# Performance work log

Measured on AMD Instinct MI355X. Metric: run time of the kernel, lower is better.

Reference implementation:

```python
import jax, jax.numpy as jnp
import numpy as np

NEG_INF = -9e15  # pygat masking constant
ALPHA = 0.2      # LeakyReLU slope


def _gat_head(h, adj_mask, W, a, concat):
    """One GraphAttentionLayer (pygat style).
    h: [b, N, Fin], adj_mask: [N, N] bool, W: [Fin, Fout], a: [2*Fout].
    """
    Fout = W.shape[1]
    Wh = jnp.einsum('bnf,fo->bno', h, W)              # [b, N, Fout]
    # e_ij = LeakyReLU(a_src . Wh_i + a_dst . Wh_j)
    e_src = Wh @ a[:Fout]                             # [b, N]
    e_dst = Wh @ a[Fout:]                             # [b, N]
    e = jax.nn.leaky_relu(e_src[:, :, None] + e_dst[:, None, :], ALPHA)  # [b, N, N]
    att = jax.nn.softmax(jnp.where(adj_mask, e, NEG_INF), axis=-1)
    out = jnp.einsum('bij,bjo->bio', att, Wh)         # [b, N, Fout]
    return jax.nn.elu(out) if concat else out


def setup_inputs() -> dict:
    key = jax.random.key(0)
    ks = jax.random.split(key, 8)
    b, N, F = 16384, 22, 192   # F = 3 * input_feature
    H = 192                    # 3 * hidden_feature (per head)
    x = jax.random.normal(ks[0], (b, N, F), dtype=jnp.float32)
    # symmetric binary adjacency with self loops (stand-in for skeleton graph A)
    u = jax.random.uniform(ks[1], (N, N))
    adj = ((u + u.T) < 0.8).astype(jnp.float32)
    adj = jnp.maximum(adj, jnp.eye(N, dtype=jnp.float32))
    s = 1.0 / np.sqrt(F)
    W1 = jax.random.normal(ks[2], (F, H), dtype=jnp.float32) * s
    a1 = jax.random.normal(ks[3], (2 * H,), dtype=jnp.float32) * s
    W2 = jax.random.normal(ks[4], (F, H), dtype=jnp.float32) * s
    a2 = jax.random.normal(ks[5], (2 * H,), dtype=jnp.float32) * s
    Wo = jax.random.normal(ks[6], (2 * H, F), dtype=jnp.float32) * (1.0 / np.sqrt(2 * H))
    ao = jax.random.normal(ks[7], (2 * F,), dtype=jnp.float32) * s
    return {"x": x, "adj": adj, "W1": W1, "a1": a1, "W2": W2, "a2": a2, "Wo": Wo, "ao": ao}


def reference(x, adj, W1, a1, W2, a2, Wo, ao):
    # ST_GCNA.forward: y = GAT(x_view, A) reshaped + residual x.
    # GAT (eval mode, dropout is identity): concat 2 heads, then elu(out_att).
    adj_mask = adj > 0
    h1 = _gat_head(x, adj_mask, W1, a1, concat=True)   # [b, N, H]
    h2 = _gat_head(x, adj_mask, W2, a2, concat=True)   # [b, N, H]
    hcat = jnp.concatenate([h1, h2], axis=-1)           # [b, N, 2H]
    y = jax.nn.elu(_gat_head(hcat, adj_mask, Wo, ao, concat=False))  # [b, N, F]
    return y + x
```

## Files before the change

kernel.cpp:

```cpp
#include <hip/hip_runtime.h>


typedef __attribute__((ext_vector_type(8))) short s16x8;
typedef __attribute__((ext_vector_type(4))) short s16x4;
typedef __attribute__((ext_vector_type(2))) int i32x2;
typedef __attribute__((ext_vector_type(4))) float f32x4;

constexpr int NN = 22;
constexpr int FF = 192;
constexpr int AS = 200;
constexpr int TS = 40;

__device__ __forceinline__ short f2bf(float f) {
  union { float f; unsigned u; } v; v.f = f;
  unsigned r = v.u + 0x7FFFu + ((v.u >> 16) & 1u);
  return (short)(r >> 16);
}

__device__ __forceinline__ int cvt_pk_bf16(float lo, float hi) {
  int r;
  asm("v_cvt_pk_bf16_f32 %0, %1, %2" : "=v"(r) : "v"(lo), "v"(hi));
  return r;
}

__device__ __forceinline__ float elu1(float v) {
  float e = __expf(v) - 1.0f;
  return v > 0.f ? v : e;
}

__global__ void prep_vec(const float* __restrict__ W1, const float* __restrict__ a1,
                         const float* __restrict__ W2, const float* __restrict__ a2,
                         const float* __restrict__ Wo, const float* __restrict__ ao,
                         float* __restrict__ vecs) {
  int t = blockIdx.x * 256 + threadIdx.x;
  if (t >= 1536) return;
  const float* W; const float* a; int k;
  if (t < 384)      { W = W1; k = t % 192;            a = a1 + (t / 192) * 192; }
  else if (t < 768) { int u = t - 384; W = W2; k = u % 192; a = a2 + (u / 192) * 192; }
  else              { int u = t - 768; W = Wo; k = u % 384; a = ao + (u / 384) * 192; }
  float s = 0.f;
  for (int o = 0; o < 192; ++o) s += W[k * 192 + o] * a[o];
  vecs[t] = s;
}

__global__ void prep_pack(const float* __restrict__ W1, const float* __restrict__ W2,
                          const float* __restrict__ Wo, const float* __restrict__ vecs,
                          short* __restrict__ dst) {
  int idx = blockIdx.x * 256 + threadIdx.x;
  const float* W; int off, ksteps, v0, v1;
  if (idx < 39936)      { W = W1; off = 0;     ksteps = 6;  v0 = 0;   v1 = 192;  }
  else if (idx < 79872) { W = W2; off = 39936; ksteps = 6;  v0 = 384; v1 = 576;  }
  else                  { W = Wo; off = 79872; ksteps = 12; v0 = 768; v1 = 1152; }
  int local = idx - off;
  int j = local & 7, l = (local >> 3) & 63, fi = local >> 9;
  int nt = fi / ksteps, ks = fi - nt * ksteps;
  int k = ks * 32 + ((l >> 4) << 3) + j;
  int nl = l & 15;
  float v;
  if (nt < 12) v = W[k * 192 + nt * 16 + nl];
  else         v = (nl == 0) ? vecs[v0 + k] : (nl == 1) ? vecs[v1 + k] : 0.f;
  dst[idx] = f2bf(v);
}

struct Accs { f32x4 a[2][3]; f32x4 e[2]; };

__device__ __forceinline__ void zacc(Accs& a) {
  #pragma unroll
  for (int m = 0; m < 2; ++m) {
    #pragma unroll
    for (int t = 0; t < 3; ++t) a.a[m][t] = (f32x4){0.f, 0.f, 0.f, 0.f};
    a.e[m] = (f32x4){0.f, 0.f, 0.f, 0.f};
  }
}

__device__ __attribute__((always_inline)) inline void gemm6(
    const short* A, const s16x8* __restrict__ B, int ksTot, int ksOff,
    Accs& ac, int m0, int kg, int wave, int lane) {
  for (int ks = 0; ks < 6; ++ks) {
    const short* ap = A + ks * 32 + kg * 8;
    s16x8 av0 = *(const s16x8*)(ap + m0 * AS);
    s16x8 av1 = *(const s16x8*)(ap + (m0 + 16) * AS);
    #pragma unroll
    for (int t = 0; t < 3; ++t) {
      s16x8 bv = B[((wave * 3 + t) * ksTot + ksOff + ks) * 64 + lane];
      ac.a[0][t] = __builtin_amdgcn_mfma_f32_16x16x32_bf16(av0, bv, ac.a[0][t], 0, 0, 0);
      ac.a[1][t] = __builtin_amdgcn_mfma_f32_16x16x32_bf16(av1, bv, ac.a[1][t], 0, 0, 0);
    }
    if (wave == 3) {
      s16x8 bv = B[(12 * ksTot + ksOff + ks) * 64 + lane];
      ac.e[0] = __builtin_amdgcn_mfma_f32_16x16x32_bf16(av0, bv, ac.e[0], 0, 0, 0);
      ac.e[1] = __builtin_amdgcn_mfma_f32_16x16x32_bf16(av1, bv, ac.e[1], 0, 0, 0);
    }
  }
}

__device__ __attribute__((always_inline)) inline void storeD(
    const Accs& ac, short* WhTp, float* esp, float* edp, int m0, int kg, int wave) {
  #pragma unroll
  for (int m = 0; m < 2; ++m)
    #pragma unroll
    for (int t = 0; t < 3; ++t) {
      int col = (wave * 3 + t) * 16 + m0;
      int row0 = m * 16 + kg * 4;
      i32x2 p = { cvt_pk_bf16(ac.a[m][t][0], ac.a[m][t][1]),
                  cvt_pk_bf16(ac.a[m][t][2], ac.a[m][t][3]) };
      *(i32x2*)&WhTp[col * TS + row0] = p;
    }
  if (wave == 3 && m0 < 2) {
    float* dst = m0 ? edp : esp;
    #pragma unroll
    for (int m = 0; m < 2; ++m) {
      int row0 = m * 16 + kg * 4;
      #pragma unroll
      for (int r = 0; r < 4; ++r)
        if (row0 + r < NN) dst[row0 + r] = ac.e[m][r];
    }
  }
}

__device__ __forceinline__ void softmax22(
    const float* es, const float* ed, const unsigned* adjm, short* attA, int tid) {
  int i = tid >> 3, jl = tid & 7;
  if (i >= NN) return;
  unsigned msk = adjm[i];
  float esi = es[i];
  float pv[3]; float mx = -3e38f;
  #pragma unroll
  for (int c = 0; c < 3; ++c) {
    int j = jl + 8 * c;
    int jc = j < NN ? j : 0;
    float e = esi + ed[jc];
    e = e > 0.f ? e : 0.2f * e;
    bool live = (j < NN) && ((msk >> j) & 1u);
    pv[c] = live ? e : -9e15f;
    mx = fmaxf(mx, pv[c]);
  }
  #pragma unroll
  for (int d = 1; d < 8; d <<= 1) mx = fmaxf(mx, __shfl_xor(mx, d, 8));
  float s = 0.f;
  #pragma unroll
  for (int c = 0; c < 3; ++c) { float q = __expf(pv[c] - mx); pv[c] = q; s += q; }
  #pragma unroll
  for (int d = 1; d < 8; d <<= 1) s += __shfl_xor(s, d, 8);
  float inv = 1.f / s;
  #pragma unroll
  for (int c = 0; c < 3; ++c) {
    int j = jl + 8 * c;
    if (j < 24) attA[i * TS + j] = (j < NN) ? f2bf(pv[c] * inv) : (short)0;
  }
  attA[i * TS + 24 + jl] = 0;
}

__device__ __attribute__((always_inline)) inline void pv22(
    const short* attAp, const short* WhTp, f32x4 pa[2][3], int m0, int kg, int wave) {
  s16x8 av0 = *(const s16x8*)(attAp + m0 * TS + kg * 8);
  s16x8 av1 = *(const s16x8*)(attAp + (m0 + 16) * TS + kg * 8);
  #pragma unroll
  for (int t = 0; t < 3; ++t) {
    int col = (wave * 3 + t) * 16 + m0;
    s16x8 bv = *(const s16x8*)(WhTp + col * TS + kg * 8);
    pa[0][t] = __builtin_amdgcn_mfma_f32_16x16x32_bf16(av0, bv, pa[0][t], 0, 0, 0);
    pa[1][t] = __builtin_amdgcn_mfma_f32_16x16x32_bf16(av1, bv, pa[1][t], 0, 0, 0);
  }
}

__global__ __launch_bounds__(256, 3) void gat_main(
    const float* __restrict__ x, const float* __restrict__ adj,
    const short* __restrict__ wsb, float* __restrict__ out) {
  __shared__ __align__(16) short As1[32 * AS];
  __shared__ __align__(16) short Ah [32 * AS];
  __shared__ __align__(16) short attA[32 * TS];
  __shared__ __align__(16) short WhT[FF * TS];
  __shared__ float es[NN], ed[NN];
  __shared__ unsigned adjm[NN];

  const int tid = threadIdx.x, lane = tid & 63, wave = tid >> 6;
  const int m0 = lane & 15, kg = (lane >> 4) & 3;
  const size_t b = blockIdx.x;
  const float* xb = x + b * (size_t)(NN * FF);

  for (int i4 = tid; i4 < 1056; i4 += 256) {
    int row = i4 / 48, c = (i4 - row * 48) * 4;
    float4 v = ((const float4*)xb)[i4];
    i32x2 p = { cvt_pk_bf16(v.x, v.y), cvt_pk_bf16(v.z, v.w) };
    *(i32x2*)&As1[row * AS + c] = p;
  }
  {
    int* z1 = (int*)(As1 + NN * AS);
    int* z2 = (int*)(Ah + NN * AS);
    for (int i = tid; i < 1000; i += 256) { z1[i] = 0; z2[i] = 0; }
  }
  if (tid < NN) {
    unsigned m = 0;
    for (int j = 0; j < NN; ++j) m |= (adj[tid * NN + j] > 0.f ? 1u : 0u) << j;
    adjm[tid] = m;
  }
  __syncthreads();

  const s16x8* BW  = (const s16x8*)wsb;
  const s16x8* BWo = (const s16x8*)wsb + 9984;

  Accs aco; zacc(aco);

  for (int h = 0; h < 2; ++h) {
    Accs ach; zacc(ach);
    gemm6(As1, BW + h * 4992, 6, 0, ach, m0, kg, wave, lane);
    storeD(ach, WhT, es, ed, m0, kg, wave);
    __syncthreads();

    softmax22(es, ed, adjm, attA, tid);
    __syncthreads();

    f32x4 pa[2][3];
    #pragma unroll
    for (int m = 0; m < 2; ++m)
      #pragma unroll
      for (int t = 0; t < 3; ++t) pa[m][t] = (f32x4){0.f, 0.f, 0.f, 0.f};
    pv22(attA, WhT, pa, m0, kg, wave);
    #pragma unroll
    for (int m = 0; m < 2; ++m)
      #pragma unroll
      for (int t = 0; t < 3; ++t) {
        int col = (wave * 3 + t) * 16 + m0;
        int row0 = m * 16 + kg * 4;
        float v0 = elu1(pa[m][t][0]), v1 = elu1(pa[m][t][1]);
        float v2 = elu1(pa[m][t][2]), v3 = elu1(pa[m][t][3]);
        int qa = cvt_pk_bf16(v0, v1), qb = cvt_pk_bf16(v2, v3);
        if (row0 < NN)     Ah[row0 * AS + col]       = (short)qa;
        if (row0 + 1 < NN) Ah[(row0 + 1) * AS + col] = (short)(qa >> 16);
        if (row0 + 2 < NN) Ah[(row0 + 2) * AS + col] = (short)qb;
        if (row0 + 3 < NN) Ah[(row0 + 3) * AS + col] = (short)(qb >> 16);
      }
    __syncthreads();

    gemm6(Ah, BWo, 12, 6 * h, aco, m0, kg, wave, lane);
  }

  storeD(aco, WhT, es, ed, m0, kg, wave);
  __syncthreads();
  softmax22(es, ed, adjm, attA, tid);
  __syncthreads();

  f32x4 pa[2][3];
  #pragma unroll
  for (int m = 0; m < 2; ++m)
    #pragma unroll
    for (int t = 0; t < 3; ++t) pa[m][t] = (f32x4){0.f, 0.f, 0.f, 0.f};
  pv22(attA, WhT, pa, m0, kg, wave);
  float* ob = out + b * (size_t)(NN * FF);
  #pragma unroll
  for (int m = 0; m < 2; ++m)
    #pragma unroll
    for (int t = 0; t < 3; ++t) {
      int col = (wave * 3 + t) * 16 + m0;
      int row0 = m * 16 + kg * 4;
      #pragma unroll
      for (int r = 0; r < 4; ++r) {
        int row = row0 + r;
        if (row < NN) {
          float v = elu1(pa[m][t][r]);
          ob[row * FF + col] = v + xb[row * FF + col];
        }
      }
    }
}

extern "C" void kernel_launch(void* const* d_in, const int* in_sizes, int n_in,
                              void* d_out, int out_size, void* d_ws, size_t ws_size,
                              hipStream_t stream) {
  const float* x   = (const float*)d_in[0];
  const float* adj = (const float*)d_in[1];
  const float* W1  = (const float*)d_in[2];
  const float* a1  = (const float*)d_in[3];
  const float* W2  = (const float*)d_in[4];
  const float* a2  = (const float*)d_in[5];
  const float* Wo  = (const float*)d_in[6];
  const float* ao  = (const float*)d_in[7];
  float* out = (float*)d_out;
  short* wsb  = (short*)d_ws;
  float* vecs = (float*)((char*)d_ws + 319488);

  const int batch = in_sizes[0] / (NN * FF);
  prep_vec <<<6,   256, 0, stream>>>(W1, a1, W2, a2, Wo, ao, vecs);
  prep_pack<<<624, 256, 0, stream>>>(W1, W2, Wo, vecs, wsb);
  gat_main <<<batch, 256, 0, stream>>>(x, adj, wsb, out);
}
```

Measured before the change: 945.2 us.

## Split row halves across eight waves with 512-thread blocks

Doubles the block size to 512 threads, with each wave computing one 16-row half of the M dimension instead of both halves. This halves the accumulators per thread and raises the number of waves per sample, which is meant to add latency hiding and MFMA issue parallelism. In exchange, every B-fragment load from global memory is now done by two waves instead of one, and the __syncthreads barriers cover more waves. Shared memory per block is unchanged, so occupancy in blocks per CU may be limited by LDS.

```diff
diff --git a/kernel.cpp b/kernel.cpp
--- a/kernel.cpp
+++ b/kernel.cpp
@@ -62,59 +62,47 @@
   dst[idx] = f2bf(v);
 }
 
-struct Accs { f32x4 a[2][3]; f32x4 e[2]; };
+struct Accs { f32x4 a[3]; f32x4 e; };
 
 __device__ __forceinline__ void zacc(Accs& a) {
   #pragma unroll
-  for (int m = 0; m < 2; ++m) {
-    #pragma unroll
-    for (int t = 0; t < 3; ++t) a.a[m][t] = (f32x4){0.f, 0.f, 0.f, 0.f};
-    a.e[m] = (f32x4){0.f, 0.f, 0.f, 0.f};
-  }
+  for (int t = 0; t < 3; ++t) a.a[t] = (f32x4){0.f, 0.f, 0.f, 0.f};
+  a.e = (f32x4){0.f, 0.f, 0.f, 0.f};
 }
 
 __device__ __attribute__((always_inline)) inline void gemm6(
     const short* A, const s16x8* __restrict__ B, int ksTot, int ksOff,
-    Accs& ac, int m0, int kg, int wave, int lane) {
+    Accs& ac, int arow, int kg, int wq, int lane) {
   for (int ks = 0; ks < 6; ++ks) {
-    const short* ap = A + ks * 32 + kg * 8;
-    s16x8 av0 = *(const s16x8*)(ap + m0 * AS);
-    s16x8 av1 = *(const s16x8*)(ap + (m0 + 16) * AS);
+    s16x8 av = *(const s16x8*)(A + arow * AS + ks * 32 + kg * 8);
     #pragma unroll
     for (int t = 0; t < 3; ++t) {
-      s16x8 bv = B[((wave * 3 + t) * ksTot + ksOff + ks) * 64 + lane];
-      ac.a[0][t] = __builtin_amdgcn_mfma_f32_16x16x32_bf16(av0, bv, ac.a[0][t], 0, 0, 0);
-      ac.a[1][t] = __builtin_amdgcn_mfma_f32_16x16x32_bf16(av1, bv, ac.a[1][t], 0, 0, 0);
-    }
-    if (wave == 3) {
+      s16x8 bv = B[((wq * 3 + t) * ksTot + ksOff + ks) * 64 + lane];
+      ac.a[t] = __builtin_amdgcn_mfma_f32_16x16x32_bf16(av, bv, ac.a[t], 0, 0, 0);
+    }
+    if (wq == 3) {
       s16x8 bv = B[(12 * ksTot + ksOff + ks) * 64 + lane];
-      ac.e[0] = __builtin_amdgcn_mfma_f32_16x16x32_bf16(av0, bv, ac.e[0], 0, 0, 0);
-      ac.e[1] = __builtin_amdgcn_mfma_f32_16x16x32_bf16(av1, bv, ac.e[1], 0, 0, 0);
+      ac.e = __builtin_amdgcn_mfma_f32_16x16x32_bf16(av, bv, ac.e, 0, 0, 0);
     }
   }
 }
 
 __device__ __attribute__((always_inline)) inline void storeD(
-    const Accs& ac, short* WhTp, float* esp, float* edp, int m0, int kg, int wave) {
-  #pragma unroll
-  for (int m = 0; m < 2; ++m)
-    #pragma unroll
-    for (int t = 0; t < 3; ++t) {
-      int col = (wave * 3 + t) * 16 + m0;
-      int row0 = m * 16 + kg * 4;
-      i32x2 p = { cvt_pk_bf16(ac.a[m][t][0], ac.a[m][t][1]),
-                  cvt_pk_bf16(ac.a[m][t][2], ac.a[m][t][3]) };
-      *(i32x2*)&WhTp[col * TS + row0] = p;
-    }
-  if (wave == 3 && m0 < 2) {
+    const Accs& ac, short* WhTp, float* esp, float* edp, int m0, int kg,
+    int wq, int mh) {
+  int row0 = mh * 16 + kg * 4;
+  #pragma unroll
+  for (int t = 0; t < 3; ++t) {
+    int col = (wq * 3 + t) * 16 + m0;
+    i32x2 p = { cvt_pk_bf16(ac.a[t][0], ac.a[t][1]),
+                cvt_pk_bf16(ac.a[t][2], ac.a[t][3]) };
+    *(i32x2*)&WhTp[col * TS + row0] = p;
+  }
+  if (wq == 3 && m0 < 2) {
     float* dst = m0 ? edp : esp;
     #pragma unroll
-    for (int m = 0; m < 2; ++m) {
-      int row0 = m * 16 + kg * 4;
-      #pragma unroll
-      for (int r = 0; r < 4; ++r)
-        if (row0 + r < NN) dst[row0 + r] = ac.e[m][r];
-    }
+    for (int r = 0; r < 4; ++r)
+      if (row0 + r < NN) dst[row0 + r] = ac.e[r];
   }
 }
 
@@ -152,19 +140,18 @@
 }
 
 __device__ __attribute__((always_inline)) inline void pv22(
-    const short* attAp, const short* WhTp, f32x4 pa[2][3], int m0, int kg, int wave) {
-  s16x8 av0 = *(const s16x8*)(attAp + m0 * TS + kg * 8);
-  s16x8 av1 = *(const s16x8*)(attAp + (m0 + 16) * TS + kg * 8);
+    const short* attAp, const short* WhTp, f32x4 pa[3], int arow, int m0,
+    int kg, int wq) {
+  s16x8 av = *(const s16x8*)(attAp + arow * TS + kg * 8);
   #pragma unroll
   for (int t = 0; t < 3; ++t) {
-    int col = (wave * 3 + t) * 16 + m0;
+    int col = (wq * 3 + t) * 16 + m0;
     s16x8 bv = *(const s16x8*)(WhTp + col * TS + kg * 8);
-    pa[0][t] = __builtin_amdgcn_mfma_f32_16x16x32_bf16(av0, bv, pa[0][t], 0, 0, 0);
-    pa[1][t] = __builtin_amdgcn_mfma_f32_16x16x32_bf16(av1, bv, pa[1][t], 0, 0, 0);
-  }
-}
-
-__global__ __launch_bounds__(256, 3) void gat_main(
+    pa[t] = __builtin_amdgcn_mfma_f32_16x16x32_bf16(av, bv, pa[t], 0, 0, 0);
+  }
+}
+
+__global__ __launch_bounds__(512, 6) void gat_main(
     const float* __restrict__ x, const float* __restrict__ adj,
     const short* __restrict__ wsb, float* __restrict__ out) {
   __shared__ __align__(16) short As1[32 * AS];
@@ -175,11 +162,13 @@
   __shared__ unsigned adjm[NN];
 
   const int tid = threadIdx.x, lane = tid & 63, wave = tid >> 6;
+  const int wq = wave & 3, mh = wave >> 2;
   const int m0 = lane & 15, kg = (lane >> 4) & 3;
+  const int arow = mh * 16 + m0;
   const size_t b = blockIdx.x;
   const float* xb = x + b * (size_t)(NN * FF);
 
-  for (int i4 = tid; i4 < 1056; i4 += 256) {
+  for (int i4 = tid; i4 < 1056; i4 += 512) {
     int row = i4 / 48, c = (i4 - row * 48) * 4;
     float4 v = ((const float4*)xb)[i4];
     i32x2 p = { cvt_pk_bf16(v.x, v.y), cvt_pk_bf16(v.z, v.w) };
@@ -188,7 +177,7 @@
   {
     int* z1 = (int*)(As1 + NN * AS);
     int* z2 = (int*)(Ah + NN * AS);
-    for (int i = tid; i < 1000; i += 256) { z1[i] = 0; z2[i] = 0; }
+    for (int i = tid; i < 1000; i += 512) { z1[i] = 0; z2[i] = 0; }
   }
   if (tid < NN) {
     unsigned m = 0;
@@ -204,65 +193,61 @@
 
   for (int h = 0; h < 2; ++h) {
     Accs ach; zacc(ach);
-    gemm6(As1, BW + h * 4992, 6, 0, ach, m0, kg, wave, lane);
-    storeD(ach, WhT, es, ed, m0, kg, wave);
+    gemm6(As1, BW + h * 4992, 6, 0, ach, arow, kg, wq, lane);
+    storeD(ach, WhT, es, ed, m0, kg, wq, mh);
     __syncthreads();
 
     softmax22(es, ed, adjm, attA, tid);
     __syncthreads();
 
-    f32x4 pa[2][3];
-    #pragma unroll
-    for (int m = 0; m < 2; ++m)
-      #pragma unroll
-      for (int t = 0; t < 3; ++t) pa[m][t] = (f32x4){0.f, 0.f, 0.f, 0.f};
-    pv22(attA, WhT, pa, m0, kg, wave);
-    #pragma unroll
-    for (int m = 0; m < 2; ++m)
+    f32x4 pa[3];
+    #pragma unroll
+    for (int t = 0; t < 3; ++t) pa[t] = (f32x4){0.f, 0.f, 0.f, 0.f};
+    pv22(attA, WhT, pa, arow, m0, kg, wq);
+    {
+      int row0 = mh * 16 + kg * 4;
       #pragma unroll
       for (int t = 0; t < 3; ++t) {
-        int col = (wave * 3 + t) * 16 + m0;
-        int row0 = m * 16 + kg * 4;
-        float v0 = elu1(pa[m][t][0]), v1 = elu1(pa[m][t][1]);
-        float v2 = elu1(pa[m][t][2]), v3 = elu1(pa[m][t][3]);
+        int col = (wq * 3 + t) * 16 + m0;
+        float v0 = elu1(pa[t][0]), v1 = elu1(pa[t][1]);
+        float v2 = elu1(pa[t][2]), v3 = elu1(pa[t][3]);
         int qa = cvt_pk_bf16(v0, v1), qb = cvt_pk_bf16(v2, v3);
         if (row0 < NN)     Ah[row0 * AS + col]       = (short)qa;
         if (row0 + 1 < NN) Ah[(row0 + 1) * AS + col] = (short)(qa >> 16);
         if (row0 + 2 < NN) Ah[(row0 + 2) * AS + col] = (short)qb;
         if (row0 + 3 < NN) Ah[(row0 + 3) * AS + col] = (short)(qb >> 16);
       }
+    }
     __syncthreads();
 
-    gemm6(Ah, BWo, 12, 6 * h, aco, m0, kg, wave, lane);
-  }
-
-  storeD(aco, WhT, es, ed, m0, kg, wave);
+    gemm6(Ah, BWo, 12, 6 * h, aco, arow, kg, wq, lane);
+  }
+
+  storeD(aco, WhT, es, ed, m0, kg, wq, mh);
   __syncthreads();
   softmax22(es, ed, adjm, attA, tid);
   __syncthreads();
 
-  f32x4 pa[2][3];
-  #pragma unroll
-  for (int m = 0; m < 2; ++m)
-    #pragma unroll
-    for (int t = 0; t < 3; ++t) pa[m][t] = (f32x4){0.f, 0.f, 0.f, 0.f};
-  pv22(attA, WhT, pa, m0, kg, wave);
+  f32x4 pa[3];
+  #pragma unroll
+  for (int t = 0; t < 3; ++t) pa[t] = (f32x4){0.f, 0.f, 0.f, 0.f};
+  pv22(attA, WhT, pa, arow, m0, kg, wq);
   float* ob = out + b * (size_t)(NN * FF);
-  #pragma unroll
-  for (int m = 0; m < 2; ++m)
+  {
+    int row0 = mh * 16 + kg * 4;
     #pragma unroll
     for (int t = 0; t < 3; ++t) {
-      int col = (wave * 3 + t) * 16 + m0;
-      int row0 = m * 16 + kg * 4;
+      int col = (wq * 3 + t) * 16 + m0;
       #pragma unroll
       for (int r = 0; r < 4; ++r) {
         int row = row0 + r;
         if (row < NN) {
-          float v = elu1(pa[m][t][r]);
+          float v = elu1(pa[t][r]);
           ob[row * FF + col] = v + xb[row * FF + col];
         }
       }
     }
+  }
 }
 
 extern "C" void kernel_launch(void* const* d_in, const int* in_sizes, int n_in,
@@ -283,5 +268,5 @@
   const int batch = in_sizes[0] / (NN * FF);
   prep_vec <<<6,   256, 0, stream>>>(W1, a1, W2, a2, Wo, ao, vecs);
   prep_pack<<<624, 256, 0, stream>>>(W1, W2, Wo, vecs, wsb);
-  gat_main <<<batch, 256, 0, stream>>>(x, adj, wsb, out);
-}
+  gat_main <<<batch, 512, 0, stream>>>(x, adj, wsb, out);
+}
```

Measured after the change: 1.296 ms. +37.1%, slower.

## Shrink LDS tiles to 23 rows and raise occupancy to five blocks per CU

Applied to the files above, without the earlier changes.

Trims the padded shared-memory buffers from 32 rows to 23, with one shared zero row. Rows 22-31 of the second MFMA tile are redirected to that zero row instead of separate zero-filled rows. The transposed Wh stride drops from 40 to 24, and launch bounds ask for five blocks per SM instead of three. The aim is to cut LDS footprint and zero-init work so more blocks stay resident. This risks register pressure under the tighter bound and relies on the WhT reads past row 24 landing on valid, correctly masked data.

```diff
diff --git a/kernel.cpp b/kernel.cpp
--- a/kernel.cpp
+++ b/kernel.cpp
@@ -9,7 +9,9 @@
 constexpr int NN = 22;
 constexpr int FF = 192;
 constexpr int AS = 200;
-constexpr int TS = 40;
+constexpr int TSA = 40;
+constexpr int TSW = 24;
+constexpr int ZROW = 22;
 
 __device__ __forceinline__ short f2bf(float f) {
   union { float f; unsigned u; } v; v.f = f;
@@ -76,10 +78,11 @@
 __device__ __attribute__((always_inline)) inline void gemm6(
     const short* A, const s16x8* __restrict__ B, int ksTot, int ksOff,
     Accs& ac, int m0, int kg, int wave, int lane) {
+  const int r1 = (m0 + 16 < NN) ? m0 + 16 : ZROW;
   for (int ks = 0; ks < 6; ++ks) {
-    const short* ap = A + ks * 32 + kg * 8;
-    s16x8 av0 = *(const s16x8*)(ap + m0 * AS);
-    s16x8 av1 = *(const s16x8*)(ap + (m0 + 16) * AS);
+    const int ko = ks * 32 + kg * 8;
+    s16x8 av0 = *(const s16x8*)(A + m0 * AS + ko);
+    s16x8 av1 = *(const s16x8*)(A + r1 * AS + ko);
     #pragma unroll
     for (int t = 0; t < 3; ++t) {
       s16x8 bv = B[((wave * 3 + t) * ksTot + ksOff + ks) * 64 + lane];
@@ -102,9 +105,11 @@
     for (int t = 0; t < 3; ++t) {
       int col = (wave * 3 + t) * 16 + m0;
       int row0 = m * 16 + kg * 4;
-      i32x2 p = { cvt_pk_bf16(ac.a[m][t][0], ac.a[m][t][1]),
-                  cvt_pk_bf16(ac.a[m][t][2], ac.a[m][t][3]) };
-      *(i32x2*)&WhTp[col * TS + row0] = p;
+      if (row0 < 24) {
+        i32x2 p = { cvt_pk_bf16(ac.a[m][t][0], ac.a[m][t][1]),
+                    cvt_pk_bf16(ac.a[m][t][2], ac.a[m][t][3]) };
+        *(i32x2*)&WhTp[col * TSW + row0] = p;
+      }
     }
   if (wave == 3 && m0 < 2) {
     float* dst = m0 ? edp : esp;
@@ -146,31 +151,32 @@
   #pragma unroll
   for (int c = 0; c < 3; ++c) {
     int j = jl + 8 * c;
-    if (j < 24) attA[i * TS + j] = (j < NN) ? f2bf(pv[c] * inv) : (short)0;
-  }
-  attA[i * TS + 24 + jl] = 0;
+    if (j < 24) attA[i * TSA + j] = (j < NN) ? f2bf(pv[c] * inv) : (short)0;
+  }
+  attA[i * TSA + 24 + jl] = 0;
 }
 
 __device__ __attribute__((always_inline)) inline void pv22(
     const short* attAp, const short* WhTp, f32x4 pa[2][3], int m0, int kg, int wave) {
-  s16x8 av0 = *(const s16x8*)(attAp + m0 * TS + kg * 8);
-  s16x8 av1 = *(const s16x8*)(attAp + (m0 + 16) * TS + kg * 8);
+  const int r1 = (m0 + 16 < NN) ? m0 + 16 : ZROW;
+  s16x8 av0 = *(const s16x8*)(attAp + m0 * TSA + kg * 8);
+  s16x8 av1 = *(const s16x8*)(attAp + r1 * TSA + kg * 8);
   #pragma unroll
   for (int t = 0; t < 3; ++t) {
     int col = (wave * 3 + t) * 16 + m0;
-    s16x8 bv = *(const s16x8*)(WhTp + col * TS + kg * 8);
+    s16x8 bv = *(const s16x8*)(WhTp + col * TSW + kg * 8);
     pa[0][t] = __builtin_amdgcn_mfma_f32_16x16x32_bf16(av0, bv, pa[0][t], 0, 0, 0);
     pa[1][t] = __builtin_amdgcn_mfma_f32_16x16x32_bf16(av1, bv, pa[1][t], 0, 0, 0);
   }
 }
 
-__global__ __launch_bounds__(256, 3) void gat_main(
+__global__ __launch_bounds__(256, 5) void gat_main(
     const float* __restrict__ x, const float* __restrict__ adj,
     const short* __restrict__ wsb, float* __restrict__ out) {
-  __shared__ __align__(16) short As1[32 * AS];
-  __shared__ __align__(16) short Ah [32 * AS];
-  __shared__ __align__(16) short attA[32 * TS];
-  __shared__ __align__(16) short WhT[FF * TS];
+  __shared__ __align__(16) short As1[23 * AS];
+  __shared__ __align__(16) short Ah [23 * AS];
+  __shared__ __align__(16) short attA[23 * TSA];
+  __shared__ __align__(16) short WhT[FF * TSW + 8];
   __shared__ float es[NN], ed[NN];
   __shared__ unsigned adjm[NN];
 
@@ -185,10 +191,11 @@
     i32x2 p = { cvt_pk_bf16(v.x, v.y), cvt_pk_bf16(v.z, v.w) };
     *(i32x2*)&As1[row * AS + c] = p;
   }
-  {
-    int* z1 = (int*)(As1 + NN * AS);
-    int* z2 = (int*)(Ah + NN * AS);
-    for (int i = tid; i < 1000; i += 256) { z1[i] = 0; z2[i] = 0; }
+  if (tid < 124) {
+    if (tid < 100)      { ((int*)(As1 + ZROW * AS))[tid] = 0;
+                          ((int*)(Ah  + ZROW * AS))[tid] = 0; }
+    else if (tid < 120) ((int*)(attA + ZROW * TSA))[tid - 100] = 0;
+    else                ((int*)(WhT + FF * TSW))[tid - 120] = 0;
   }
   if (tid < NN) {
     unsigned m = 0;
```

After: 1.171 ms. 23.9% more time.
